# Optimization experiments

Measured on AMD Instinct MI355X. Metric: run time of the kernel, lower is better.

The kernel has to match this reference:

```python
import jax, jax.numpy as jnp
import numpy as np

NUM_ACTIONS = 16  # number of unique leaf actions (= output_dim)


def setup_inputs() -> dict:
    key = jax.random.key(0)
    ks = jax.random.split(key, 7)
    B, IN, D, A = 32768, 128, 511, 512
    L = D + A + 1  # 1024 leaves
    x = jax.random.normal(ks[0], (B, IN), dtype=jnp.float32)
    Wd = jax.random.normal(ks[1], (D, IN), dtype=jnp.float32) * 0.05
    bd = jax.random.normal(ks[2], (D,), dtype=jnp.float32) * 0.05
    Wa = jax.random.normal(ks[3], (A, IN), dtype=jnp.float32) * 0.05
    ba = jax.random.normal(ks[4], (A,), dtype=jnp.float32) * 0.05
    Wl = jax.random.normal(ks[5], (L, 2 * (D + A)), dtype=jnp.float32) * 0.05
    seg_ids = jax.random.randint(ks[6], (L,), 0, NUM_ACTIONS, dtype=jnp.int32)
    return {"x": x, "Wd": Wd, "bd": bd, "Wa": Wa, "ba": ba, "Wl": Wl,
            "seg_ids": seg_ids}


def reference(x, Wd, bd, Wa, ba, Wl, seg_ids):
    # dual linear heads (torch Linear: y = x @ W.T + b)
    x1 = x @ Wd.T + bd            # [B, D]
    x2 = x @ Wa.T + ba            # [B, A]
    h = jnp.concatenate([x1, x2], axis=1)                     # [B, D+A]
    hh = jnp.concatenate([jax.nn.relu(h), jax.nn.relu(-h)], axis=1)  # [B, 2(D+A)]
    leaf = hh @ Wl.T              # [B, L]
    # ragged per-action max over leaf columns (MaxPoolLayer)
    pooled = jax.ops.segment_max(leaf.T, seg_ids,
                                 num_segments=NUM_ACTIONS).T   # [B, NUM_ACTIONS]
    return jax.nn.softmax(pooled, axis=-1)
```

## Files before the change

### kernel.cpp

```cpp
#include <hip/hip_runtime.h>
#include <hip/hip_bf16.h>
#include <cstdint>
#include <cmath>

#define AS1 __attribute__((address_space(1)))
#define AS3 __attribute__((address_space(3)))

typedef unsigned short u16;
typedef uint32_t u32;
typedef __attribute__((ext_vector_type(8))) __bf16 bf16x8;
typedef __attribute__((ext_vector_type(8))) unsigned short u16x8;
typedef __attribute__((ext_vector_type(4))) float f32x4;

__device__ __forceinline__ u16 f2bf(float f) {
    uint32_t u = __builtin_bit_cast(uint32_t, f);
    return (u16)((u + 0x7fffu + ((u >> 16) & 1u)) >> 16);
}

__device__ __forceinline__ u32 f2ord(float f) {
    u32 u = __builtin_bit_cast(u32, f);
    return u ^ (u32)(((int32_t)u >> 31) | 0x80000000);
}
__device__ __forceinline__ float ord2f(u32 v) {
    u32 u = (v & 0x80000000u) ? (v ^ 0x80000000u) : ~v;
    return __builtin_bit_cast(float, u);
}


__global__ void setup_all(const float* __restrict__ x,
                          const float* __restrict__ Wd, const float* __restrict__ bd,
                          const float* __restrict__ Wa, const float* __restrict__ ba,
                          const float* __restrict__ Wl,
                          u16* __restrict__ xb, u16* __restrict__ w1b,
                          float* __restrict__ bb, u16* __restrict__ w1t,
                          u16* __restrict__ wsb, u16* __restrict__ dlb,
                          float* __restrict__ cl) {
    __shared__ float cred[256];
    const int b = blockIdx.x;
    const int tid = threadIdx.x;
    if (b < 2048) {
        long idx = (long)(b * 256 + tid) * 8;
        float4 a = *(const float4*)(x + idx);
        float4 c = *(const float4*)(x + idx + 4);
        u16x8 o;
        o[0]=f2bf(a.x); o[1]=f2bf(a.y); o[2]=f2bf(a.z); o[3]=f2bf(a.w);
        o[4]=f2bf(c.x); o[5]=f2bf(c.y); o[6]=f2bf(c.z); o[7]=f2bf(c.w);
        *(u16x8*)(xb + idx) = o;
    } else if (b < 2112) {
        int t = (b - 2048) * 256 + tid;
        int row = t >> 4, g = (t & 15) * 8;
        const float* src = nullptr;
        if (row < 511)       src = Wd + row * 128 + g;
        else if (row < 1023) src = Wa + (row - 511) * 128 + g;
        u16x8 o = 0;
        if (src) {
            #pragma unroll
            for (int j = 0; j < 8; ++j) o[j] = f2bf(src[j]);
        }
        *(u16x8*)(w1b + row * 128 + g) = o;
        #pragma unroll
        for (int j = 0; j < 8; ++j) w1t[(g + j) * 1024 + row] = o[j];
        if ((t & 15) == 0)
            bb[row] = row < 511 ? bd[row] : (row < 1023 ? ba[row - 511] : 0.f);
    } else {
        const int l0 = (b - 2112) * 2;
        const int lo = tid >> 7, g = (tid & 127) * 8;
        const float* src = Wl + (long)(l0 + lo) * 2046;
        u16x8 os, od;
        float part = 0.f;
        #pragma unroll
        for (int j = 0; j < 8; ++j) {
            int c = g + j;
            float pa = 0.f, pb = 0.f;
            if (c < 1023) { pa = src[c]; pb = src[1023 + c]; }
            os[j] = f2bf(0.5f * (pa + pb));
            float v = pa - pb;
            od[j] = f2bf(v);
            float b1 = c < 511 ? bd[c] : (c < 1023 ? ba[c - 511] : 0.f);
            part += v * b1;
        }
        *(u16x8*)(wsb + (long)(l0 + lo) * 1024 + g) = os;
        *(u16x8*)(dlb + (long)(l0 + lo) * 1024 + g) = od;
        cred[tid] = part;
        __syncthreads();
        if (tid < 2) {
            float s = 0.f;
            #pragma unroll
            for (int k = 0; k < 128; ++k) s += cred[tid * 128 + k];
            cl[l0 + tid] = 0.5f * s;
        }
    }
}

__global__ __launch_bounds__(256) void gemm_hwc(
        const u16* __restrict__ xb, const u16* __restrict__ w1b,
        const float* __restrict__ bb,
        const u16* __restrict__ dlb, const u16* __restrict__ w1t,
        u16* __restrict__ habs, u16* __restrict__ wcb) {
    __shared__ union SharedU {
        struct { u16 As[2][4096]; u16 Bs[2][4096]; } s;
        u16 obuf[128 * 132];
    } sh;
    const int tid  = threadIdx.x;
    const int lane = tid & 63, wave = tid >> 6;
    const int wy = wave >> 1, wx = wave & 1;
    const int i16 = lane & 15, q = lane >> 4;
    const int cA = wave * 2, srow = lane >> 2;
    const int scol = (((lane & 3) ^ ((lane >> 3) & 3))) * 8;
    const int qa   = (q ^ ((i16 >> 1) & 3)) * 8;

    f32x4 acc[4][4];
    #pragma unroll
    for (int m = 0; m < 4; ++m)
        #pragma unroll
        for (int n = 0; n < 4; ++n) acc[m][n] = f32x4{0.f,0.f,0.f,0.f};

    if (blockIdx.y == 0) {
        const long blockM = (long)blockIdx.x * 128;
        const int koff = (blockIdx.x * 4) & 31;
        const u16* a0 = dlb + (blockM + cA * 16 + srow) * 1024 + scol;
        const u16* a1 = dlb + (blockM + (cA + 1) * 16 + srow) * 1024 + scol;
        const u16* b0 = w1t + (long)(cA * 16 + srow) * 1024 + scol;
        const u16* b1 = w1t + (long)((cA + 1) * 16 + srow) * 1024 + scol;
        for (int it = 0; it < 32; ++it) {
            const int k0 = ((it + koff) & 31) << 5;
            __builtin_amdgcn_global_load_lds((const AS1 void*)(a0 + k0), (AS3 void*)&sh.s.As[0][cA * 512],       16, 0, 0);
            __builtin_amdgcn_global_load_lds((const AS1 void*)(a1 + k0), (AS3 void*)&sh.s.As[0][(cA + 1) * 512], 16, 0, 0);
            __builtin_amdgcn_global_load_lds((const AS1 void*)(b0 + k0), (AS3 void*)&sh.s.Bs[0][cA * 512],       16, 0, 0);
            __builtin_amdgcn_global_load_lds((const AS1 void*)(b1 + k0), (AS3 void*)&sh.s.Bs[0][(cA + 1) * 512], 16, 0, 0);
            __syncthreads();
            bf16x8 af[4], bfv[4];
            #pragma unroll
            for (int s = 0; s < 4; ++s) {
                af[s]  = *(const bf16x8*)&sh.s.As[0][(wy * 64 + s * 16 + i16) * 32 + qa];
                bfv[s] = *(const bf16x8*)&sh.s.Bs[0][(wx * 64 + s * 16 + i16) * 32 + qa];
            }
            #pragma unroll
            for (int sm = 0; sm < 4; ++sm)
                #pragma unroll
                for (int sn = 0; sn < 4; ++sn)
                    acc[sm][sn] = __builtin_amdgcn_mfma_f32_16x16x32_bf16(af[sm], bfv[sn], acc[sm][sn], 0, 0, 0);
            __syncthreads();
        }
        #pragma unroll
        for (int sm = 0; sm < 4; ++sm)
            #pragma unroll
            for (int sn = 0; sn < 4; ++sn) {
                const int col = wx * 64 + sn * 16 + i16;
                #pragma unroll
                for (int r = 0; r < 4; ++r) {
                    const long row = blockM + wy * 64 + sm * 16 + 4 * q + r;
                    wcb[row * 128 + col] = f2bf(0.5f * acc[sm][sn][r]);
                }
            }
        return;
    }

    const int xcd = blockIdx.x, yy = blockIdx.y - 1;
    const long blockM = (long)(xcd * 32 + (yy >> 3)) * 128;
    const int  blockN = (yy & 7) * 128;
    const int  koff = (yy >> 3) & 1;

    const u16* a0 = xb + (blockM + cA * 16 + srow) * 128 + scol;
    const u16* a1 = xb + (blockM + (cA + 1) * 16 + srow) * 128 + scol;
    const u16* b0 = w1b + ((long)blockN + cA * 16 + srow) * 128 + scol;
    const u16* b1 = w1b + ((long)blockN + (cA + 1) * 16 + srow) * 128 + scol;
    for (int it = 0; it < 2; ++it) {
        const int k0 = ((it + koff) & 1) << 6;
        #pragma unroll
        for (int p = 0; p < 2; ++p) {
            const int kp = k0 + p * 32;
            __builtin_amdgcn_global_load_lds((const AS1 void*)(a0 + kp), (AS3 void*)&sh.s.As[p][cA * 512],       16, 0, 0);
            __builtin_amdgcn_global_load_lds((const AS1 void*)(a1 + kp), (AS3 void*)&sh.s.As[p][(cA + 1) * 512], 16, 0, 0);
            __builtin_amdgcn_global_load_lds((const AS1 void*)(b0 + kp), (AS3 void*)&sh.s.Bs[p][cA * 512],       16, 0, 0);
            __builtin_amdgcn_global_load_lds((const AS1 void*)(b1 + kp), (AS3 void*)&sh.s.Bs[p][(cA + 1) * 512], 16, 0, 0);
        }
        __syncthreads();
        #pragma unroll
        for (int p = 0; p < 2; ++p) {
            bf16x8 af[4], bfv[4];
            #pragma unroll
            for (int s = 0; s < 4; ++s) {
                af[s]  = *(const bf16x8*)&sh.s.As[p][(wy * 64 + s * 16 + i16) * 32 + qa];
                bfv[s] = *(const bf16x8*)&sh.s.Bs[p][(wx * 64 + s * 16 + i16) * 32 + qa];
            }
            #pragma unroll
            for (int sm = 0; sm < 4; ++sm)
                #pragma unroll
                for (int sn = 0; sn < 4; ++sn)
                    acc[sm][sn] = __builtin_amdgcn_mfma_f32_16x16x32_bf16(af[sm], bfv[sn], acc[sm][sn], 0, 0, 0);
        }
        __syncthreads();
    }

    float bv[4];
    #pragma unroll
    for (int sn = 0; sn < 4; ++sn) bv[sn] = bb[blockN + wx * 64 + sn * 16 + i16];
    #pragma unroll
    for (int sm = 0; sm < 4; ++sm)
        #pragma unroll
        for (int sn = 0; sn < 4; ++sn)
            #pragma unroll
            for (int r = 0; r < 4; ++r)
                sh.obuf[(wy * 64 + sm * 16 + 4 * q + r) * 132 + wx * 64 + sn * 16 + i16] =
                    f2bf(fabsf(acc[sm][sn][r] + bv[sn]));
    __syncthreads();
    const int cg = (tid & 15) * 8;
    #pragma unroll
    for (int it = 0; it < 8; ++it) {
        const int row = it * 16 + (tid >> 4);
        *(u16x8*)&habs[(blockM + row) * 1024 + blockN + cg] =
            *(const u16x8*)&sh.obuf[row * 132 + cg];
    }
}

__global__ __launch_bounds__(512, 2) void gemm_leaf(const u16* __restrict__ habs,
        const u16* __restrict__ xb, const u16* __restrict__ wsb,
        const u16* __restrict__ wcb, const float* __restrict__ cl,
        const int* __restrict__ seg, u32* __restrict__ pp) {
    __shared__ __align__(16) u16 As[4][256 * 32];
    __shared__ __align__(16) u16 Bs[4][256 * 32];
    __shared__ u32 pmax[256 * 16];
    const int tid  = threadIdx.x;
    const int lane = tid & 63, w = tid >> 6;
    const int wm = w >> 2, wn = w & 3;
    const int i16 = lane & 15, q = lane >> 4;

    const int bid  = blockIdx.x;
    const int wgid = (bid & 7) * 64 + (bid >> 3);
    const int mT = wgid >> 2, nT = wgid & 3;
    const long blockM = (long)mT * 256;
    const int  blockN = nT * 256;

    #pragma unroll
    for (int j = 0; j < 8; ++j) pmax[tid + j * 512] = 0u;

    const int r0 = tid >> 2;
    const int scol = (((tid & 3) ^ ((tid >> 3) & 3))) * 8;
    const u16* gA1 = habs + (blockM + r0) * 1024 + scol;
    const u16* gB1 = wsb  + (long)(blockN + r0) * 1024 + scol;
    const u16* gA2 = xb   + (blockM + r0) * 128 + scol;
    const u16* gB2 = wcb  + (long)(blockN + r0) * 128 + scol;
    const int ldsb = w * 512;

    auto stageA = [&](int tt) {
        u16* dst = &As[tt & 3][ldsb];
        const u16* g; int jstr;
        if (tt < 32) { g = gA1 + tt * 32;        jstr = 128 * 1024; }
        else         { g = gA2 + (tt - 32) * 32; jstr = 128 * 128; }
        __builtin_amdgcn_global_load_lds((const AS1 void*)g,          (AS3 void*)dst,          16, 0, 0);
        __builtin_amdgcn_global_load_lds((const AS1 void*)(g + jstr), (AS3 void*)(dst + 4096), 16, 0, 0);
    };
    auto stageB = [&](int tt) {
        u16* dst = &Bs[tt & 3][ldsb];
        const u16* g; int jstr;
        if (tt < 32) { g = gB1 + tt * 32;        jstr = 128 * 1024; }
        else         { g = gB2 + (tt - 32) * 32; jstr = 128 * 128; }
        __builtin_amdgcn_global_load_lds((const AS1 void*)g,          (AS3 void*)dst,          16, 0, 0);
        __builtin_amdgcn_global_load_lds((const AS1 void*)(g + jstr), (AS3 void*)(dst + 4096), 16, 0, 0);
    };

    f32x4 acc[8][4];
    #pragma unroll
    for (int m = 0; m < 8; ++m)
        #pragma unroll
        for (int n = 0; n < 4; ++n) acc[m][n] = f32x4{0.f,0.f,0.f,0.f};
    bf16x8 areg[4], breg[4];

    const int rdc = (q ^ ((i16 >> 1) & 3)) * 8;
    auto lda = [&](int slot, int mh) {
        #pragma unroll
        for (int mf = 0; mf < 4; ++mf)
            areg[mf] = *(const bf16x8*)&As[slot][(wm * 128 + mh * 64 + mf * 16 + i16) * 32 + rdc];
    };
    auto ldb = [&](int slot) {
        #pragma unroll
        for (int nf = 0; nf < 4; ++nf)
            breg[nf] = *(const bf16x8*)&Bs[slot][(wn * 64 + nf * 16 + i16) * 32 + rdc];
    };
    auto mf16 = [&](int mh) {
        #pragma unroll
        for (int mf = 0; mf < 4; ++mf)
            #pragma unroll
            for (int nf = 0; nf < 4; ++nf)
                acc[mh * 4 + mf][nf] = __builtin_amdgcn_mfma_f32_16x16x32_bf16(
                    areg[mf], breg[nf], acc[mh * 4 + mf][nf], 0, 0, 0);
    };

    stageA(0); stageB(0); stageA(1); stageB(1);
    asm volatile("s_waitcnt vmcnt(4)" ::: "memory");
    __builtin_amdgcn_s_barrier();

    for (int t = 0; t < 36; ++t) {
        const int slot = t & 3;
        lda(slot, 0); ldb(slot);
        if (t + 2 < 36) stageA(t + 2);
        __builtin_amdgcn_s_barrier();
        asm volatile("s_waitcnt lgkmcnt(0)" ::: "memory");
        __builtin_amdgcn_sched_barrier(0);
        __builtin_amdgcn_s_setprio(1);
        mf16(0);
        __builtin_amdgcn_s_setprio(0);
        __builtin_amdgcn_s_barrier();
        lda(slot, 1);
        if (t + 2 < 36) stageB(t + 2);
        __builtin_amdgcn_s_barrier();
        asm volatile("s_waitcnt lgkmcnt(0)" ::: "memory");
        __builtin_amdgcn_sched_barrier(0);
        __builtin_amdgcn_s_setprio(1);
        mf16(1);
        __builtin_amdgcn_s_setprio(0);
        if (t < 34)       { asm volatile("s_waitcnt vmcnt(4)" ::: "memory"); }
        else if (t == 34) { asm volatile("s_waitcnt vmcnt(0)" ::: "memory"); }
        __builtin_amdgcn_s_barrier();
    }

    int segc[4]; float clv[4];
    #pragma unroll
    for (int nf = 0; nf < 4; ++nf) {
        const int col = blockN + wn * 64 + nf * 16 + i16;
        segc[nf] = seg[col];
        clv[nf]  = cl[col];
    }
    #pragma unroll
    for (int mf = 0; mf < 8; ++mf)
        #pragma unroll
        for (int nf = 0; nf < 4; ++nf)
            #pragma unroll
            for (int r = 0; r < 4; ++r) {
                const int rl = wm * 128 + mf * 16 + 4 * q + r;
                atomicMax(&pmax[rl * 16 + segc[nf]], f2ord(acc[mf][nf][r] + clv[nf]));
            }
    __syncthreads();
    #pragma unroll
    for (int j = 0; j < 8; ++j) {
        int idx = tid + j * 512;
        pp[((long)nT << 19) + ((blockM + (idx >> 4)) << 4) + (idx & 15)] = pmax[idx];
    }
}

__global__ __launch_bounds__(256) void finalize(const u32* __restrict__ pp,
                                                float* __restrict__ out) {
    const int tid = threadIdx.x;
    const long row = (long)blockIdx.x * 16 + (tid >> 4);
    const int t = tid & 15;
    u32 m = 0;
    #pragma unroll
    for (int p = 0; p < 4; ++p)
        m = max(m, pp[((long)p << 19) + (row << 4) + t]);
    float logit = ord2f(m);
    float rm = logit;
    #pragma unroll
    for (int d = 8; d >= 1; d >>= 1) rm = fmaxf(rm, __shfl_xor(rm, d, 16));
    float e = __expf(logit - rm);
    float s = e;
    #pragma unroll
    for (int d = 8; d >= 1; d >>= 1) s += __shfl_xor(s, d, 16);
    out[(row << 4) + t] = e / s;
}

extern "C" void kernel_launch(void* const* d_in, const int* in_sizes, int n_in,
                              void* d_out, int out_size, void* d_ws, size_t ws_size,
                              hipStream_t stream) {
    const float* x  = (const float*)d_in[0];
    const float* Wd = (const float*)d_in[1];
    const float* bd = (const float*)d_in[2];
    const float* Wa = (const float*)d_in[3];
    const float* ba = (const float*)d_in[4];
    const float* Wl = (const float*)d_in[5];
    const int*  seg = (const int*)d_in[6];
    float* out = (float*)d_out;

    char* ws = (char*)d_ws;
    u16*   xb   = (u16*)(ws);
    u16*   w1b  = (u16*)(ws + 8388608);
    float* bb   = (float*)(ws + 8650752);
    u16*   w1t  = (u16*)(ws + 8654848);
    u16*   wsb  = (u16*)(ws + 8916992);
    u16*   dlb  = (u16*)(ws + 11014144);
    u16*   wcb  = (u16*)(ws + 13111296);
    float* clp  = (float*)(ws + 13373440);
    u16*   habs = (u16*)(ws + 13377536);
    u32*   pp   = (u32*)(ws + 80486400);

    setup_all<<<2624, 256, 0, stream>>>(x, Wd, bd, Wa, ba, Wl,
                                        xb, w1b, bb, w1t, wsb, dlb, clp);
    gemm_hwc <<<dim3(8, 257), 256, 0, stream>>>(xb, w1b, bb, dlb, w1t, habs, wcb);
    gemm_leaf<<<dim3(512), 512, 0, stream>>>(habs, xb, wsb, wcb, clp, seg, pp);
    finalize <<<2048, 256, 0, stream>>>(pp, out);
}
```

Measured before the change: 207.1 us.

## Collapse leaf GEMM inner-loop barriers and merge per-N partial maxima via global atomics

```diff
diff --git a/kernel.cpp b/kernel.cpp
--- a/kernel.cpp
+++ b/kernel.cpp
@@ -34,7 +34,7 @@
                           u16* __restrict__ xb, u16* __restrict__ w1b,
                           float* __restrict__ bb, u16* __restrict__ w1t,
                           u16* __restrict__ wsb, u16* __restrict__ dlb,
-                          float* __restrict__ cl) {
+                          float* __restrict__ cl, u32* __restrict__ pooled) {
     __shared__ float cred[256];
     const int b = blockIdx.x;
     const int tid = threadIdx.x;
@@ -62,7 +62,7 @@
         for (int j = 0; j < 8; ++j) w1t[(g + j) * 1024 + row] = o[j];
         if ((t & 15) == 0)
             bb[row] = row < 511 ? bd[row] : (row < 1023 ? ba[row - 511] : 0.f);
-    } else {
+    } else if (b < 2624) {
         const int l0 = (b - 2112) * 2;
         const int lo = tid >> 7, g = (tid & 127) * 8;
         const float* src = Wl + (long)(l0 + lo) * 2046;
@@ -89,6 +89,12 @@
             for (int k = 0; k < 128; ++k) s += cred[tid * 128 + k];
             cl[l0 + tid] = 0.5f * s;
         }
+    } else {
+        uint4* p4 = (uint4*)pooled;
+        const int base = (b - 2624) * 16384;
+        #pragma unroll
+        for (int j = 0; j < 64; ++j)
+            p4[base + tid + j * 256] = uint4{0u, 0u, 0u, 0u};
     }
 }
 
@@ -217,7 +223,7 @@
 __global__ __launch_bounds__(512, 2) void gemm_leaf(const u16* __restrict__ habs,
         const u16* __restrict__ xb, const u16* __restrict__ wsb,
         const u16* __restrict__ wcb, const float* __restrict__ cl,
-        const int* __restrict__ seg, u32* __restrict__ pp) {
+        const int* __restrict__ seg, u32* __restrict__ pooled) {
     __shared__ __align__(16) u16 As[4][256 * 32];
     __shared__ __align__(16) u16 Bs[4][256 * 32];
     __shared__ u32 pmax[256 * 16];
@@ -265,26 +271,26 @@
     for (int m = 0; m < 8; ++m)
         #pragma unroll
         for (int n = 0; n < 4; ++n) acc[m][n] = f32x4{0.f,0.f,0.f,0.f};
-    bf16x8 areg[4], breg[4];
+    bf16x8 areg0[4], areg1[4], breg[4];
 
     const int rdc = (q ^ ((i16 >> 1) & 3)) * 8;
-    auto lda = [&](int slot, int mh) {
+    auto lda = [&](bf16x8* ar, int slot, int mh) {
         #pragma unroll
         for (int mf = 0; mf < 4; ++mf)
-            areg[mf] = *(const bf16x8*)&As[slot][(wm * 128 + mh * 64 + mf * 16 + i16) * 32 + rdc];
+            ar[mf] = *(const bf16x8*)&As[slot][(wm * 128 + mh * 64 + mf * 16 + i16) * 32 + rdc];
     };
     auto ldb = [&](int slot) {
         #pragma unroll
         for (int nf = 0; nf < 4; ++nf)
             breg[nf] = *(const bf16x8*)&Bs[slot][(wn * 64 + nf * 16 + i16) * 32 + rdc];
     };
-    auto mf16 = [&](int mh) {
+    auto mf16 = [&](const bf16x8* ar, int mh) {
         #pragma unroll
         for (int mf = 0; mf < 4; ++mf)
             #pragma unroll
             for (int nf = 0; nf < 4; ++nf)
                 acc[mh * 4 + mf][nf] = __builtin_amdgcn_mfma_f32_16x16x32_bf16(
-                    areg[mf], breg[nf], acc[mh * 4 + mf][nf], 0, 0, 0);
+                    ar[mf], breg[nf], acc[mh * 4 + mf][nf], 0, 0, 0);
     };
 
     stageA(0); stageB(0); stageA(1); stageB(1);
@@ -293,22 +299,17 @@
 
     for (int t = 0; t < 36; ++t) {
         const int slot = t & 3;
-        lda(slot, 0); ldb(slot);
-        if (t + 2 < 36) stageA(t + 2);
-        __builtin_amdgcn_s_barrier();
+        lda(areg0, slot, 0); ldb(slot); lda(areg1, slot, 1);
+        if (t + 2 < 36) { stageA(t + 2); stageB(t + 2); }
+        asm volatile("s_waitcnt lgkmcnt(4)" ::: "memory");
+        __builtin_amdgcn_sched_barrier(0);
+        __builtin_amdgcn_s_setprio(1);
+        mf16(areg0, 0);
+        __builtin_amdgcn_s_setprio(0);
         asm volatile("s_waitcnt lgkmcnt(0)" ::: "memory");
         __builtin_amdgcn_sched_barrier(0);
         __builtin_amdgcn_s_setprio(1);
-        mf16(0);
-        __builtin_amdgcn_s_setprio(0);
-        __builtin_amdgcn_s_barrier();
-        lda(slot, 1);
-        if (t + 2 < 36) stageB(t + 2);
-        __builtin_amdgcn_s_barrier();
-        asm volatile("s_waitcnt lgkmcnt(0)" ::: "memory");
-        __builtin_amdgcn_sched_barrier(0);
-        __builtin_amdgcn_s_setprio(1);
-        mf16(1);
+        mf16(areg1, 1);
         __builtin_amdgcn_s_setprio(0);
         if (t < 34)       { asm volatile("s_waitcnt vmcnt(4)" ::: "memory"); }
         else if (t == 34) { asm volatile("s_waitcnt vmcnt(0)" ::: "memory"); }
@@ -335,20 +336,16 @@
     #pragma unroll
     for (int j = 0; j < 8; ++j) {
         int idx = tid + j * 512;
-        pp[((long)nT << 19) + ((blockM + (idx >> 4)) << 4) + (idx & 15)] = pmax[idx];
-    }
-}
-
-__global__ __launch_bounds__(256) void finalize(const u32* __restrict__ pp,
+        atomicMax(&pooled[((blockM + (idx >> 4)) << 4) + (idx & 15)], pmax[idx]);
+    }
+}
+
+__global__ __launch_bounds__(256) void finalize(const u32* __restrict__ pooled,
                                                 float* __restrict__ out) {
     const int tid = threadIdx.x;
     const long row = (long)blockIdx.x * 16 + (tid >> 4);
     const int t = tid & 15;
-    u32 m = 0;
-    #pragma unroll
-    for (int p = 0; p < 4; ++p)
-        m = max(m, pp[((long)p << 19) + (row << 4) + t]);
-    float logit = ord2f(m);
+    float logit = ord2f(pooled[(row << 4) + t]);
     float rm = logit;
     #pragma unroll
     for (int d = 8; d >= 1; d >>= 1) rm = fmaxf(rm, __shfl_xor(rm, d, 16));
@@ -381,11 +378,11 @@
     u16*   wcb  = (u16*)(ws + 13111296);
     float* clp  = (float*)(ws + 13373440);
     u16*   habs = (u16*)(ws + 13377536);
-    u32*   pp   = (u32*)(ws + 80486400);
-
-    setup_all<<<2624, 256, 0, stream>>>(x, Wd, bd, Wa, ba, Wl,
-                                        xb, w1b, bb, w1t, wsb, dlb, clp);
+    u32*   pooled = (u32*)(ws + 80486400);
+
+    setup_all<<<2632, 256, 0, stream>>>(x, Wd, bd, Wa, ba, Wl,
+                                        xb, w1b, bb, w1t, wsb, dlb, clp, pooled);
     gemm_hwc <<<dim3(8, 257), 256, 0, stream>>>(xb, w1b, bb, dlb, w1t, habs, wcb);
-    gemm_leaf<<<dim3(512), 512, 0, stream>>>(habs, xb, wsb, wcb, clp, seg, pp);
-    finalize <<<2048, 256, 0, stream>>>(pp, out);
-}
+    gemm_leaf<<<dim3(512), 512, 0, stream>>>(habs, xb, wsb, wcb, clp, seg, pooled);
+    finalize <<<2048, 256, 0, stream>>>(pooled, out);
+}
```

Measured after the change: 199.8 us. 3.5% less time.
